# Kernel tuning notes

Measured on AMD Instinct MI355X. Metric: run time of the kernel, lower is better.

## Reference

```python
import jax, jax.numpy as jnp
import numpy as np

S = 1
R = 64
INV_T = 100.0
EVAL_STEPS = 7  # module in eval mode
EPS = 1e-6


def setup_inputs() -> dict:
    key = jax.random.key(0)
    kx, kb = jax.random.split(key)
    B, C, H, W = 8, 512, 64, 64
    x = jax.random.uniform(kx, (B, C, H, W), dtype=jnp.float32)  # non-negative input for NMF
    bases = jax.random.uniform(kb, (B * S, C // S, R), dtype=jnp.float32)
    # F.normalize(bases, dim=1): L2-normalize along D
    bases = bases / jnp.linalg.norm(bases, axis=1, keepdims=True)
    return {"x": x, "bases": bases}


def reference(x, bases):
    B, C, H, W = x.shape
    D = C // S
    N = H * W
    xf = x.reshape(B * S, D, N)  # (BS, D, N)

    # initial coefficients: softmax(inv_t * x^T @ bases)
    coef = jax.nn.softmax(INV_T * jnp.einsum('bdn,bdr->bnr', xf, bases), axis=-1)

    def mu_step(carry, _):
        bases, coef = carry
        # update coef: coef *= (x^T bases) / (coef (bases^T bases) + eps)
        num = jnp.einsum('bdn,bdr->bnr', xf, bases)            # (BS, N, R)
        gram_b = jnp.einsum('bdr,bds->brs', bases, bases)      # (BS, R, R)
        coef = coef * num / (jnp.einsum('bnr,brs->bns', coef, gram_b) + EPS)
        # update bases: bases *= (x coef) / (bases (coef^T coef) + eps)
        num_b = jnp.einsum('bdn,bnr->bdr', xf, coef)           # (BS, D, R)
        gram_c = jnp.einsum('bnr,bns->brs', coef, coef)        # (BS, R, R)
        bases = bases * num_b / (jnp.einsum('bdr,brs->bds', bases, gram_c) + EPS)
        return (bases, coef), None

    (bases, coef), _ = jax.lax.scan(mu_step, (bases, coef), None, length=EVAL_STEPS)

    # compute_coef: one extra coef multiplicative update
    num = jnp.einsum('bdn,bdr->bnr', xf, bases)
    gram_b = jnp.einsum('bdr,bds->brs', bases, bases)
    coef = coef * num / (jnp.einsum('bnr,brs->bns', coef, gram_b) + EPS)

    out = jnp.einsum('bdr,bnr->bdn', bases, coef)  # bases @ coef^T
    return out.reshape(B, C, H, W)
```

## Files before the change

kernel.cpp:

```cpp
#include <hip/hip_runtime.h>
#include <math.h>

#define BATCH 8
#define DD 512
#define NN 4096
#define RR 64
#define NSTEPS 7
#define INV_T 100.0f
#define EPSV 1e-6f

typedef __attribute__((ext_vector_type(8))) _Float16 f16x8;
typedef __attribute__((ext_vector_type(4))) _Float16 f16x4;
typedef __attribute__((ext_vector_type(4))) float f32x4;

__device__ __forceinline__ _Float16 f2h(float f) { return (_Float16)f; }

__global__ __launch_bounds__(256) void xcvt_kernel(
    const float* __restrict__ x, _Float16* __restrict__ x_h,
    _Float16* __restrict__ xT_h) {
  __shared__ _Float16 t[64][72];
  const int n0 = blockIdx.x * 64, d0 = blockIdx.y * 64, b = blockIdx.z;
  const int tid = threadIdx.x;
  const size_t xbase = (size_t)(b * DD + d0) * NN + n0;
#pragma unroll
  for (int i = 0; i < 4; ++i) {
    const int idx = tid + i * 256;
    const int row = idx >> 4, c4 = (idx & 15) * 4;
    const float4 v = *(const float4*)(x + xbase + (size_t)row * NN + c4);
    f16x4 hv = {f2h(v.x), f2h(v.y), f2h(v.z), f2h(v.w)};
    *(f16x4*)(x_h + xbase + (size_t)row * NN + c4) = hv;
    *(f16x4*)&t[row][c4] = hv;
  }
  __syncthreads();
  const size_t tbase = (size_t)(b * NN + n0) * DD + d0;
#pragma unroll
  for (int i = 0; i < 4; ++i) {
    const int idx = tid + i * 256;
    const int row = idx >> 4, c4 = (idx & 15) * 4;
    f16x4 w = {t[c4][row], t[c4 + 1][row], t[c4 + 2][row], t[c4 + 3][row]};
    *(f16x4*)(xT_h + tbase + (size_t)row * DD + c4) = w;
  }
}

__global__ __launch_bounds__(256) void bases_prep_kernel(
    const float* __restrict__ bin, float* __restrict__ bases,
    _Float16* __restrict__ bases_h, _Float16* __restrict__ basesT_h) {
  __shared__ float t[64][65];
  const int d0 = blockIdx.x * 64, b = blockIdx.y;
  const int tid = threadIdx.x;
  const size_t base = (size_t)(b * DD + d0) * RR;
#pragma unroll
  for (int i = 0; i < 4; ++i) {
    const int idx = tid + i * 256;
    const int row = idx >> 4, c4 = (idx & 15) * 4;
    const float4 v = *(const float4*)(bin + base + row * RR + c4);
    *(float4*)(bases + base + row * RR + c4) = v;
    f16x4 hv = {f2h(v.x), f2h(v.y), f2h(v.z), f2h(v.w)};
    *(f16x4*)(bases_h + base + row * RR + c4) = hv;
    t[row][c4] = v.x; t[row][c4 + 1] = v.y; t[row][c4 + 2] = v.z; t[row][c4 + 3] = v.w;
  }
  __syncthreads();
#pragma unroll
  for (int i = 0; i < 4; ++i) {
    const int idx = tid + i * 256;
    const int row = idx >> 4, c4 = (idx & 15) * 4;
    f16x4 w = {f2h(t[c4][row]), f2h(t[c4 + 1][row]), f2h(t[c4 + 2][row]),
               f2h(t[c4 + 3][row])};
    *(f16x4*)(basesT_h + (size_t)(b * RR + row) * DD + d0 + c4) = w;
  }
}

__global__ __launch_bounds__(256) void gramT_kernel(
    const _Float16* __restrict__ T, float* __restrict__ pg, int K, int ksl) {
  const int sp = blockIdx.x, b = blockIdx.y;
  const int tid = threadIdx.x;
  const int w = tid >> 6, l = tid & 63, lo = l & 15, hi = l >> 4;
  const int k0 = sp * ksl;
  const _Float16* ap = T + (size_t)(b * RR + w * 16 + lo) * K + k0 + hi * 8;
  const _Float16* bp = T + (size_t)(b * RR + lo) * K + k0 + hi * 8;
  f32x4 acc[4] = {};
  for (int ks = 0; ks < ksl; ks += 32) {
    f16x8 a = *(const f16x8*)(ap + ks);
#pragma unroll
    for (int c = 0; c < 4; ++c) {
      f16x8 bb = *(const f16x8*)(bp + (size_t)c * 16 * K + ks);
      acc[c] = __builtin_amdgcn_mfma_f32_16x16x32_f16(a, bb, acc[c], 0, 0, 0);
    }
  }
  float* op = pg + ((size_t)(b * gridDim.x + sp) * RR + w * 16 + hi * 4) * RR;
#pragma unroll
  for (int c = 0; c < 4; ++c)
#pragma unroll
    for (int r = 0; r < 4; ++r) op[r * RR + c * 16 + lo] = acc[c][r];
}

__global__ __launch_bounds__(256) void greduce2_kernel(
    const float* __restrict__ pg, int S, float* __restrict__ g32,
    _Float16* __restrict__ ghf) {
  const int idx = blockIdx.x * 256 + threadIdx.x;
  const int b = idx >> 12, e = idx & 4095;
  const float* p = pg + (size_t)(b * S) * 4096 + e;
  float s = 0.f;
  for (int c = 0; c < S; ++c) s += p[(size_t)c * 4096];
  g32[idx] = s;
  ghf[idx] = f2h(s);
}

template <int MODE>
__global__ __launch_bounds__(256) void coef_update_kernel(
    const _Float16* __restrict__ xT_h, const _Float16* __restrict__ basesT_h,
    const _Float16* __restrict__ gram_b_h, float* __restrict__ coef,
    _Float16* __restrict__ coef_h, _Float16* __restrict__ coefT_h) {
  const int nt = blockIdx.x, b = blockIdx.y;
  const int tid = threadIdx.x;
  const int w = tid >> 6, l = tid & 63, lo = l & 15, hi = l >> 4;
  const int n0 = nt * 64;

  const _Float16* ap = xT_h + (size_t)(b * NN + n0 + w * 16 + lo) * DD + hi * 8;
  const _Float16* bp = basesT_h + (size_t)(b * RR + lo) * DD + hi * 8;
  f32x4 acc[4] = {};
#pragma unroll
  for (int ks = 0; ks < 16; ++ks) {
    f16x8 a = *(const f16x8*)(ap + ks * 32);
#pragma unroll
    for (int c = 0; c < 4; ++c) {
      f16x8 bb = *(const f16x8*)(bp + (size_t)c * 16 * DD + ks * 32);
      acc[c] = __builtin_amdgcn_mfma_f32_16x16x32_f16(a, bb, acc[c], 0, 0, 0);
    }
  }

  float v[4][4];
  float* cp = coef + (size_t)(b * NN + n0 + w * 16 + hi * 4) * RR;

  if (MODE == 0) {
#pragma unroll
    for (int reg = 0; reg < 4; ++reg) {
      float m = fmaxf(fmaxf(acc[0][reg], acc[1][reg]),
                      fmaxf(acc[2][reg], acc[3][reg]));
      m = fmaxf(m, __shfl_xor(m, 1));
      m = fmaxf(m, __shfl_xor(m, 2));
      m = fmaxf(m, __shfl_xor(m, 4));
      m = fmaxf(m, __shfl_xor(m, 8));
      float s = 0.f, e[4];
#pragma unroll
      for (int c = 0; c < 4; ++c) {
        e[c] = expf(INV_T * (acc[c][reg] - m));
        s += e[c];
      }
      s += __shfl_xor(s, 1);
      s += __shfl_xor(s, 2);
      s += __shfl_xor(s, 4);
      s += __shfl_xor(s, 8);
      const float inv = 1.f / s;
#pragma unroll
      for (int c = 0; c < 4; ++c) v[c][reg] = e[c] * inv;
    }
  } else {
    const _Float16* dap = coef_h + (size_t)(b * NN + n0 + w * 16 + lo) * RR + hi * 8;
    f32x4 den[4] = {};
#pragma unroll
    for (int kk = 0; kk < 2; ++kk) {
      f16x8 a = *(const f16x8*)(dap + kk * 32);
#pragma unroll
      for (int c = 0; c < 4; ++c) {
        f16x8 g = *(const f16x8*)(gram_b_h + (size_t)(b * RR + c * 16 + lo) * RR +
                                  kk * 32 + hi * 8);
        den[c] = __builtin_amdgcn_mfma_f32_16x16x32_f16(a, g, den[c], 0, 0, 0);
      }
    }
#pragma unroll
    for (int reg = 0; reg < 4; ++reg)
#pragma unroll
      for (int c = 0; c < 4; ++c) {
        const float oldc = cp[reg * RR + c * 16 + lo];
        v[c][reg] = oldc * acc[c][reg] / (den[c][reg] + EPSV);
      }
  }

#pragma unroll
  for (int reg = 0; reg < 4; ++reg)
#pragma unroll
    for (int c = 0; c < 4; ++c) {
      cp[reg * RR + c * 16 + lo] = v[c][reg];
      coef_h[(size_t)(b * NN + n0 + w * 16 + hi * 4 + reg) * RR + c * 16 + lo] =
          f2h(v[c][reg]);
    }
#pragma unroll
  for (int c = 0; c < 4; ++c) {
    f16x4 t4 = {f2h(v[c][0]), f2h(v[c][1]), f2h(v[c][2]), f2h(v[c][3])};
    *(f16x4*)(coefT_h + (size_t)(b * RR + c * 16 + lo) * NN + n0 + w * 16 + hi * 4) = t4;
  }
}

__global__ __launch_bounds__(256) void numb_kernel(
    const _Float16* __restrict__ x_h, const _Float16* __restrict__ coefT_h,
    float* __restrict__ pnb) {
  const int kc = blockIdx.x, dt = blockIdx.y, b = blockIdx.z;
  const int tid = threadIdx.x;
  const int w = tid >> 6, l = tid & 63, lo = l & 15, hi = l >> 4;
  const _Float16* ap =
      x_h + (size_t)(b * DD + dt * 64 + w * 16 + lo) * NN + kc * 1024 + hi * 8;
  const _Float16* bp = coefT_h + (size_t)(b * RR + lo) * NN + kc * 1024 + hi * 8;
  f32x4 acc[4] = {};
#pragma unroll 4
  for (int ks = 0; ks < 32; ++ks) {
    f16x8 a = *(const f16x8*)(ap + ks * 32);
#pragma unroll
    for (int c = 0; c < 4; ++c) {
      f16x8 bb = *(const f16x8*)(bp + (size_t)c * 16 * NN + ks * 32);
      acc[c] = __builtin_amdgcn_mfma_f32_16x16x32_f16(a, bb, acc[c], 0, 0, 0);
    }
  }
  float* op = pnb + ((size_t)((b * 4 + kc) * DD) + dt * 64 + w * 16 + hi * 4) * RR;
#pragma unroll
  for (int c = 0; c < 4; ++c)
#pragma unroll
    for (int r = 0; r < 4; ++r) op[r * RR + c * 16 + lo] = acc[c][r];
}

__global__ __launch_bounds__(256) void bases_update_kernel(
    const float* __restrict__ pnb, const float* __restrict__ gram_c,
    float* __restrict__ bases, _Float16* __restrict__ bases_h,
    _Float16* __restrict__ basesT_h) {
  __shared__ float bsm[64 * 65];
  __shared__ float gs[64 * 64];
  const int dt = blockIdx.x, b = blockIdx.y;
  float* bg = bases + (size_t)(b * DD + dt * 64) * RR;
  const int tid = threadIdx.x, tx = tid & 15, ty = tid >> 4;
  for (int idx = tid; idx < 4096; idx += 256) {
    const int row = idx >> 6, cc = idx & 63;
    bsm[row * 65 + cc] = bg[row * 64 + cc];
  }
  const float* gcp = gram_c + (size_t)b * 4096;
  for (int idx = tid; idx < 1024; idx += 256)
    *(float4*)&gs[idx * 4] = *(const float4*)(gcp + idx * 4);
  __syncthreads();

  float nb[4][4];
#pragma unroll
  for (int i = 0; i < 4; ++i) {
    float4 s = make_float4(0.f, 0.f, 0.f, 0.f);
#pragma unroll
    for (int kc = 0; kc < 4; ++kc) {
      const float4 vv = *(const float4*)(pnb +
          (((size_t)b * 4 + kc) * DD + dt * 64 + ty * 4 + i) * RR + tx * 4);
      s.x += vv.x; s.y += vv.y; s.z += vv.z; s.w += vv.w;
    }
    nb[i][0] = s.x; nb[i][1] = s.y; nb[i][2] = s.z; nb[i][3] = s.w;
  }

  float den[4][4] = {};
  for (int s = 0; s < 64; ++s) {
    float a[4];
#pragma unroll
    for (int i = 0; i < 4; ++i) a[i] = bsm[(ty * 4 + i) * 65 + s];
    const float4 gv = *(float4*)&gs[s * 64 + tx * 4];
    const float g4[4] = {gv.x, gv.y, gv.z, gv.w};
#pragma unroll
    for (int i = 0; i < 4; ++i)
#pragma unroll
      for (int j = 0; j < 4; ++j) den[i][j] = fmaf(a[i], g4[j], den[i][j]);
  }

  float v[4][4];
#pragma unroll
  for (int i = 0; i < 4; ++i) {
    float4 vv;
#pragma unroll
    for (int j = 0; j < 4; ++j) {
      const float oldb = bsm[(ty * 4 + i) * 65 + tx * 4 + j];
      v[i][j] = oldb * nb[i][j] / (den[i][j] + EPSV);
    }
    vv.x = v[i][0]; vv.y = v[i][1]; vv.z = v[i][2]; vv.w = v[i][3];
    *(float4*)&bg[(ty * 4 + i) * 64 + tx * 4] = vv;
    f16x4 bv = {f2h(v[i][0]), f2h(v[i][1]), f2h(v[i][2]), f2h(v[i][3])};
    *(f16x4*)(bases_h + (size_t)(b * DD + dt * 64 + ty * 4 + i) * RR + tx * 4) = bv;
  }
#pragma unroll
  for (int j = 0; j < 4; ++j) {
    f16x4 tv = {f2h(v[0][j]), f2h(v[1][j]), f2h(v[2][j]), f2h(v[3][j])};
    *(f16x4*)(basesT_h + (size_t)(b * RR + tx * 4 + j) * DD + dt * 64 + ty * 4) = tv;
  }
}

__global__ __launch_bounds__(256) void out_kernel(
    const _Float16* __restrict__ bases_h, const _Float16* __restrict__ coef_h,
    float* __restrict__ out) {
  const int nt = blockIdx.x, dt = blockIdx.y, b = blockIdx.z;
  const int tid = threadIdx.x;
  const int w = tid >> 6, l = tid & 63, lo = l & 15, hi = l >> 4;
  const int n0 = nt * 64;
  const _Float16* ap =
      bases_h + (size_t)(b * DD + dt * 64 + w * 16 + lo) * RR + hi * 8;
  f32x4 acc[4] = {};
#pragma unroll
  for (int kk = 0; kk < 2; ++kk) {
    f16x8 a = *(const f16x8*)(ap + kk * 32);
#pragma unroll
    for (int c = 0; c < 4; ++c) {
      f16x8 bb = *(const f16x8*)(coef_h + (size_t)(b * NN + n0 + c * 16 + lo) * RR +
                                 kk * 32 + hi * 8);
      acc[c] = __builtin_amdgcn_mfma_f32_16x16x32_f16(a, bb, acc[c], 0, 0, 0);
    }
  }
  float* op = out + (size_t)(b * DD + dt * 64 + w * 16 + hi * 4) * NN + n0;
#pragma unroll
  for (int c = 0; c < 4; ++c)
#pragma unroll
    for (int r = 0; r < 4; ++r) op[(size_t)r * NN + c * 16 + lo] = acc[c][r];
}

extern "C" void kernel_launch(void* const* d_in, const int* in_sizes, int n_in,
                              void* d_out, int out_size, void* d_ws,
                              size_t ws_size, hipStream_t stream) {
  (void)in_sizes; (void)n_in; (void)out_size; (void)ws_size;
  const float* x = (const float*)d_in[0];
  const float* bases_in = (const float*)d_in[1];

  float* W = (float*)d_ws;
  size_t o = 0;
  float* coef = W + o;     o += (size_t)BATCH * NN * RR;
  float* bases = W + o;    o += (size_t)BATCH * DD * RR;
  float* gram_b32 = W + o; o += (size_t)BATCH * 4096;
  float* gram_c32 = W + o; o += (size_t)BATCH * 4096;
  float* pnb = W + o;      o += (size_t)BATCH * 4 * DD * RR;
  float* pgram = W + o;    o += (size_t)BATCH * 16 * 4096;
  _Float16* U = (_Float16*)(W + o);
  size_t u = 0;
  _Float16* coef_h = U + u;   u += (size_t)BATCH * NN * RR;
  _Float16* coefT_h = U + u;  u += (size_t)BATCH * NN * RR;
  _Float16* bases_h = U + u;  u += (size_t)BATCH * DD * RR;
  _Float16* basesT_h = U + u; u += (size_t)BATCH * DD * RR;
  _Float16* gram_b_h = U + u; u += (size_t)BATCH * 4096;
  _Float16* gram_c_h = U + u; u += (size_t)BATCH * 4096;

  _Float16* xT_h = (_Float16*)d_out;
  _Float16* x_h = xT_h + (size_t)BATCH * NN * DD;

  xcvt_kernel<<<dim3(64, 8, BATCH), 256, 0, stream>>>(x, x_h, xT_h);
  bases_prep_kernel<<<dim3(8, BATCH), 256, 0, stream>>>(bases_in, bases, bases_h,
                                                        basesT_h);
  gramT_kernel<<<dim3(4, BATCH), 256, 0, stream>>>(basesT_h, pgram, DD, 128);
  greduce2_kernel<<<128, 256, 0, stream>>>(pgram, 4, gram_b32, gram_b_h);

  coef_update_kernel<0><<<dim3(64, BATCH), 256, 0, stream>>>(
      xT_h, basesT_h, gram_b_h, coef, coef_h, coefT_h);

  for (int step = 0; step < NSTEPS; ++step) {
    coef_update_kernel<1><<<dim3(64, BATCH), 256, 0, stream>>>(
        xT_h, basesT_h, gram_b_h, coef, coef_h, coefT_h);
    gramT_kernel<<<dim3(16, BATCH), 256, 0, stream>>>(coefT_h, pgram, NN, 256);
    greduce2_kernel<<<128, 256, 0, stream>>>(pgram, 16, gram_c32, gram_c_h);
    numb_kernel<<<dim3(4, 8, BATCH), 256, 0, stream>>>(x_h, coefT_h, pnb);
    bases_update_kernel<<<dim3(8, BATCH), 256, 0, stream>>>(pnb, gram_c32, bases,
                                                            bases_h, basesT_h);
    gramT_kernel<<<dim3(4, BATCH), 256, 0, stream>>>(basesT_h, pgram, DD, 128);
    greduce2_kernel<<<128, 256, 0, stream>>>(pgram, 4, gram_b32, gram_b_h);
  }

  coef_update_kernel<1><<<dim3(64, BATCH), 256, 0, stream>>>(
      xT_h, basesT_h, gram_b_h, coef, coef_h, coefT_h);

  out_kernel<<<dim3(64, 8, BATCH), 256, 0, stream>>>(bases_h, coef_h, (float*)d_out);
}
```

Measured before the change: 638.2 us.

## Fuse NMF pipeline into a persistent cooperative kernel with grid syncs

```diff
diff --git a/kernel.cpp b/kernel.cpp
--- a/kernel.cpp
+++ b/kernel.cpp
@@ -1,5 +1,8 @@
 #include <hip/hip_runtime.h>
+#include <hip/hip_cooperative_groups.h>
 #include <math.h>
+
+namespace cg = cooperative_groups;
 
 #define BATCH 8
 #define DD 512
@@ -8,6 +11,10 @@
 #define NSTEPS 7
 #define INV_T 100.0f
 #define EPSV 1e-6f
+#define GRID 512
+#define SMEMB 24832
+#define GC_SCALE (1.0f / 1024.0f)
+#define GC_UNSCALE 1024.0f
 
 typedef __attribute__((ext_vector_type(8))) _Float16 f16x8;
 typedef __attribute__((ext_vector_type(4))) _Float16 f16x4;
@@ -15,13 +22,12 @@
 
 __device__ __forceinline__ _Float16 f2h(float f) { return (_Float16)f; }
 
-__global__ __launch_bounds__(256) void xcvt_kernel(
-    const float* __restrict__ x, _Float16* __restrict__ x_h,
-    _Float16* __restrict__ xT_h) {
-  __shared__ _Float16 t[64][72];
-  const int n0 = blockIdx.x * 64, d0 = blockIdx.y * 64, b = blockIdx.z;
-  const int tid = threadIdx.x;
+__device__ __forceinline__ void do_xcvt(const float* x, _Float16* x_h,
+                                        _Float16* xT_h, int b, int d0, int n0,
+                                        int tid, char* smem) {
+  _Float16(*t)[72] = (_Float16(*)[72])smem;
   const size_t xbase = (size_t)(b * DD + d0) * NN + n0;
+  __syncthreads();
 #pragma unroll
   for (int i = 0; i < 4; ++i) {
     const int idx = tid + i * 256;
@@ -37,24 +43,24 @@
   for (int i = 0; i < 4; ++i) {
     const int idx = tid + i * 256;
     const int row = idx >> 4, c4 = (idx & 15) * 4;
-    f16x4 w = {t[c4][row], t[c4 + 1][row], t[c4 + 2][row], t[c4 + 3][row]};
-    *(f16x4*)(xT_h + tbase + (size_t)row * DD + c4) = w;
-  }
-}
-
-__global__ __launch_bounds__(256) void bases_prep_kernel(
-    const float* __restrict__ bin, float* __restrict__ bases,
-    _Float16* __restrict__ bases_h, _Float16* __restrict__ basesT_h) {
-  __shared__ float t[64][65];
-  const int d0 = blockIdx.x * 64, b = blockIdx.y;
-  const int tid = threadIdx.x;
+    f16x4 wv = {t[c4][row], t[c4 + 1][row], t[c4 + 2][row], t[c4 + 3][row]};
+    *(f16x4*)(xT_h + tbase + (size_t)row * DD + c4) = wv;
+  }
+}
+
+__device__ __forceinline__ void do_bases_prep(const float* bin, float* bases32,
+                                              _Float16* bases_h,
+                                              _Float16* basesT_h, int b, int d0,
+                                              int tid, char* smem) {
+  float(*t)[65] = (float(*)[65])smem;
   const size_t base = (size_t)(b * DD + d0) * RR;
+  __syncthreads();
 #pragma unroll
   for (int i = 0; i < 4; ++i) {
     const int idx = tid + i * 256;
     const int row = idx >> 4, c4 = (idx & 15) * 4;
     const float4 v = *(const float4*)(bin + base + row * RR + c4);
-    *(float4*)(bases + base + row * RR + c4) = v;
+    *(float4*)(bases32 + base + row * RR + c4) = v;
     f16x4 hv = {f2h(v.x), f2h(v.y), f2h(v.z), f2h(v.w)};
     *(f16x4*)(bases_h + base + row * RR + c4) = hv;
     t[row][c4] = v.x; t[row][c4 + 1] = v.y; t[row][c4 + 2] = v.z; t[row][c4 + 3] = v.w;
@@ -64,58 +70,57 @@
   for (int i = 0; i < 4; ++i) {
     const int idx = tid + i * 256;
     const int row = idx >> 4, c4 = (idx & 15) * 4;
-    f16x4 w = {f2h(t[c4][row]), f2h(t[c4 + 1][row]), f2h(t[c4 + 2][row]),
-               f2h(t[c4 + 3][row])};
-    *(f16x4*)(basesT_h + (size_t)(b * RR + row) * DD + d0 + c4) = w;
-  }
-}
-
-__global__ __launch_bounds__(256) void gramT_kernel(
-    const _Float16* __restrict__ T, float* __restrict__ pg, int K, int ksl) {
-  const int sp = blockIdx.x, b = blockIdx.y;
-  const int tid = threadIdx.x;
-  const int w = tid >> 6, l = tid & 63, lo = l & 15, hi = l >> 4;
-  const int k0 = sp * ksl;
-  const _Float16* ap = T + (size_t)(b * RR + w * 16 + lo) * K + k0 + hi * 8;
-  const _Float16* bp = T + (size_t)(b * RR + lo) * K + k0 + hi * 8;
+    f16x4 wv = {f2h(t[c4][row]), f2h(t[c4 + 1][row]), f2h(t[c4 + 2][row]),
+                f2h(t[c4 + 3][row])};
+    *(f16x4*)(basesT_h + (size_t)(b * RR + row) * DD + d0 + c4) = wv;
+  }
+}
+
+__device__ __forceinline__ void do_gramb_init(const _Float16* basesT_h,
+                                              float* pgb, int b, int tid, int w,
+                                              int lo, int hi) {
+  const _Float16* ap = basesT_h + (size_t)(b * RR + w * 16 + lo) * DD + hi * 8;
+  const _Float16* bp = basesT_h + (size_t)(b * RR + lo) * DD + hi * 8;
   f32x4 acc[4] = {};
-  for (int ks = 0; ks < ksl; ks += 32) {
-    f16x8 a = *(const f16x8*)(ap + ks);
+#pragma unroll
+  for (int ks = 0; ks < 16; ++ks) {
+    f16x8 a = *(const f16x8*)(ap + ks * 32);
 #pragma unroll
     for (int c = 0; c < 4; ++c) {
-      f16x8 bb = *(const f16x8*)(bp + (size_t)c * 16 * K + ks);
+      f16x8 bb = *(const f16x8*)(bp + (size_t)c * 16 * DD + ks * 32);
       acc[c] = __builtin_amdgcn_mfma_f32_16x16x32_f16(a, bb, acc[c], 0, 0, 0);
     }
   }
-  float* op = pg + ((size_t)(b * gridDim.x + sp) * RR + w * 16 + hi * 4) * RR;
+  float* op = pgb + (size_t)(b * 8) * 4096;
 #pragma unroll
   for (int c = 0; c < 4; ++c)
 #pragma unroll
-    for (int r = 0; r < 4; ++r) op[r * RR + c * 16 + lo] = acc[c][r];
-}
-
-__global__ __launch_bounds__(256) void greduce2_kernel(
-    const float* __restrict__ pg, int S, float* __restrict__ g32,
-    _Float16* __restrict__ ghf) {
-  const int idx = blockIdx.x * 256 + threadIdx.x;
-  const int b = idx >> 12, e = idx & 4095;
-  const float* p = pg + (size_t)(b * S) * 4096 + e;
-  float s = 0.f;
-  for (int c = 0; c < S; ++c) s += p[(size_t)c * 4096];
-  g32[idx] = s;
-  ghf[idx] = f2h(s);
+    for (int r = 0; r < 4; ++r)
+      op[(w * 16 + hi * 4 + r) * RR + c * 16 + lo] = acc[c][r];
+  for (int sp = 1; sp < 8; ++sp)
+    for (int idx = tid; idx < 4096; idx += 256)
+      pgb[(size_t)(b * 8 + sp) * 4096 + idx] = 0.f;
 }
 
 template <int MODE>
-__global__ __launch_bounds__(256) void coef_update_kernel(
-    const _Float16* __restrict__ xT_h, const _Float16* __restrict__ basesT_h,
-    const _Float16* __restrict__ gram_b_h, float* __restrict__ coef,
-    _Float16* __restrict__ coef_h, _Float16* __restrict__ coefT_h) {
-  const int nt = blockIdx.x, b = blockIdx.y;
-  const int tid = threadIdx.x;
-  const int w = tid >> 6, l = tid & 63, lo = l & 15, hi = l >> 4;
+__device__ __forceinline__ void do_coef(const _Float16* xT_h,
+                                        const _Float16* basesT_h,
+                                        const float* pgb, float* coef32,
+                                        _Float16* coef_h, _Float16* coefT_h,
+                                        int b, int nt, int tid, int w, int lo,
+                                        int hi, char* smem) {
+  _Float16* gsm = (_Float16*)smem;
+  if (MODE == 1) {
+    __syncthreads();
+    for (int idx = tid; idx < 4096; idx += 256) {
+      float s = 0.f;
+#pragma unroll
+      for (int sp = 0; sp < 8; ++sp)
+        s += pgb[(size_t)(b * 8 + sp) * 4096 + idx];
+      gsm[idx] = f2h(s);
+    }
+  }
   const int n0 = nt * 64;
-
   const _Float16* ap = xT_h + (size_t)(b * NN + n0 + w * 16 + lo) * DD + hi * 8;
   const _Float16* bp = basesT_h + (size_t)(b * RR + lo) * DD + hi * 8;
   f32x4 acc[4] = {};
@@ -130,7 +135,7 @@
   }
 
   float v[4][4];
-  float* cp = coef + (size_t)(b * NN + n0 + w * 16 + hi * 4) * RR;
+  float* cp = coef32 + (size_t)(b * NN + n0 + w * 16 + hi * 4) * RR;
 
   if (MODE == 0) {
 #pragma unroll
@@ -156,6 +161,7 @@
       for (int c = 0; c < 4; ++c) v[c][reg] = e[c] * inv;
     }
   } else {
+    __syncthreads();
     const _Float16* dap = coef_h + (size_t)(b * NN + n0 + w * 16 + lo) * RR + hi * 8;
     f32x4 den[4] = {};
 #pragma unroll
@@ -163,9 +169,8 @@
       f16x8 a = *(const f16x8*)(dap + kk * 32);
 #pragma unroll
       for (int c = 0; c < 4; ++c) {
-        f16x8 g = *(const f16x8*)(gram_b_h + (size_t)(b * RR + c * 16 + lo) * RR +
-                                  kk * 32 + hi * 8);
-        den[c] = __builtin_amdgcn_mfma_f32_16x16x32_f16(a, g, den[c], 0, 0, 0);
+        f16x8 gv = *(const f16x8*)(gsm + (c * 16 + lo) * RR + kk * 32 + hi * 8);
+        den[c] = __builtin_amdgcn_mfma_f32_16x16x32_f16(a, gv, den[c], 0, 0, 0);
       }
     }
 #pragma unroll
@@ -192,12 +197,10 @@
   }
 }
 
-__global__ __launch_bounds__(256) void numb_kernel(
-    const _Float16* __restrict__ x_h, const _Float16* __restrict__ coefT_h,
-    float* __restrict__ pnb) {
-  const int kc = blockIdx.x, dt = blockIdx.y, b = blockIdx.z;
-  const int tid = threadIdx.x;
-  const int w = tid >> 6, l = tid & 63, lo = l & 15, hi = l >> 4;
+__device__ __forceinline__ void do_numb(const _Float16* x_h,
+                                        const _Float16* coefT_h, float* pnb,
+                                        int kc, int dt, int b, int w, int lo,
+                                        int hi) {
   const _Float16* ap =
       x_h + (size_t)(b * DD + dt * 64 + w * 16 + lo) * NN + kc * 1024 + hi * 8;
   const _Float16* bp = coefT_h + (size_t)(b * RR + lo) * NN + kc * 1024 + hi * 8;
@@ -218,22 +221,49 @@
     for (int r = 0; r < 4; ++r) op[r * RR + c * 16 + lo] = acc[c][r];
 }
 
-__global__ __launch_bounds__(256) void bases_update_kernel(
-    const float* __restrict__ pnb, const float* __restrict__ gram_c,
-    float* __restrict__ bases, _Float16* __restrict__ bases_h,
-    _Float16* __restrict__ basesT_h) {
-  __shared__ float bsm[64 * 65];
-  __shared__ float gs[64 * 64];
-  const int dt = blockIdx.x, b = blockIdx.y;
-  float* bg = bases + (size_t)(b * DD + dt * 64) * RR;
-  const int tid = threadIdx.x, tx = tid & 15, ty = tid >> 4;
+__device__ __forceinline__ void do_gramc(const _Float16* coefT_h, float* pgram,
+                                         int sp, int b, int w, int lo, int hi) {
+  const int k0 = sp * 256;
+  const _Float16* ap = coefT_h + (size_t)(b * RR + w * 16 + lo) * NN + k0 + hi * 8;
+  const _Float16* bp = coefT_h + (size_t)(b * RR + lo) * NN + k0 + hi * 8;
+  f32x4 acc[4] = {};
+#pragma unroll
+  for (int ks = 0; ks < 8; ++ks) {
+    f16x8 a = *(const f16x8*)(ap + ks * 32);
+#pragma unroll
+    for (int c = 0; c < 4; ++c) {
+      f16x8 bb = *(const f16x8*)(bp + (size_t)c * 16 * NN + ks * 32);
+      acc[c] = __builtin_amdgcn_mfma_f32_16x16x32_f16(a, bb, acc[c], 0, 0, 0);
+    }
+  }
+  float* op = pgram + ((size_t)(b * 16 + sp) * RR + w * 16 + hi * 4) * RR;
+#pragma unroll
+  for (int c = 0; c < 4; ++c)
+#pragma unroll
+    for (int r = 0; r < 4; ++r) op[r * RR + c * 16 + lo] = acc[c][r];
+}
+
+__device__ __forceinline__ void do_bases_upd(const float* pnb,
+                                             const float* pgram, float* bases32,
+                                             _Float16* bases_h,
+                                             _Float16* basesT_h, float* pgb,
+                                             int dt, int b, int tid, int tx,
+                                             int ty, char* smem) {
+  float* bsm = (float*)smem;
+  _Float16* gsh = (_Float16*)(smem + 16640);
+  float* bg = bases32 + (size_t)(b * DD + dt * 64) * RR;
+  __syncthreads();
   for (int idx = tid; idx < 4096; idx += 256) {
     const int row = idx >> 6, cc = idx & 63;
     bsm[row * 65 + cc] = bg[row * 64 + cc];
   }
-  const float* gcp = gram_c + (size_t)b * 4096;
-  for (int idx = tid; idx < 1024; idx += 256)
-    *(float4*)&gs[idx * 4] = *(const float4*)(gcp + idx * 4);
+  for (int idx = tid; idx < 4096; idx += 256) {
+    float s = 0.f;
+#pragma unroll
+    for (int sp = 0; sp < 16; ++sp)
+      s += pgram[(size_t)(b * 16 + sp) * 4096 + idx];
+    gsh[idx] = f2h(s * GC_SCALE);
+  }
   __syncthreads();
 
   float nb[4][4];
@@ -254,8 +284,8 @@
     float a[4];
 #pragma unroll
     for (int i = 0; i < 4; ++i) a[i] = bsm[(ty * 4 + i) * 65 + s];
-    const float4 gv = *(float4*)&gs[s * 64 + tx * 4];
-    const float g4[4] = {gv.x, gv.y, gv.z, gv.w};
+    const f16x4 gv = *(const f16x4*)&gsh[s * 64 + tx * 4];
+    const float g4[4] = {(float)gv[0], (float)gv[1], (float)gv[2], (float)gv[3]};
 #pragma unroll
     for (int i = 0; i < 4; ++i)
 #pragma unroll
@@ -269,7 +299,7 @@
 #pragma unroll
     for (int j = 0; j < 4; ++j) {
       const float oldb = bsm[(ty * 4 + i) * 65 + tx * 4 + j];
-      v[i][j] = oldb * nb[i][j] / (den[i][j] + EPSV);
+      v[i][j] = oldb * nb[i][j] / fmaf(den[i][j], GC_UNSCALE, EPSV);
     }
     vv.x = v[i][0]; vv.y = v[i][1]; vv.z = v[i][2]; vv.w = v[i][3];
     *(float4*)&bg[(ty * 4 + i) * 64 + tx * 4] = vv;
@@ -281,14 +311,37 @@
     f16x4 tv = {f2h(v[0][j]), f2h(v[1][j]), f2h(v[2][j]), f2h(v[3][j])};
     *(f16x4*)(basesT_h + (size_t)(b * RR + tx * 4 + j) * DD + dt * 64 + ty * 4) = tv;
   }
-}
-
-__global__ __launch_bounds__(256) void out_kernel(
-    const _Float16* __restrict__ bases_h, const _Float16* __restrict__ coef_h,
-    float* __restrict__ out) {
-  const int nt = blockIdx.x, dt = blockIdx.y, b = blockIdx.z;
-  const int tid = threadIdx.x;
-  const int w = tid >> 6, l = tid & 63, lo = l & 15, hi = l >> 4;
+  __syncthreads();
+#pragma unroll
+  for (int i = 0; i < 4; ++i)
+#pragma unroll
+    for (int j = 0; j < 4; ++j) bsm[(ty * 4 + i) * 65 + tx * 4 + j] = v[i][j];
+  __syncthreads();
+
+  float pa[4][4] = {};
+  for (int d = 0; d < 64; ++d) {
+    float a[4], bb[4];
+#pragma unroll
+    for (int i = 0; i < 4; ++i) a[i] = bsm[d * 65 + ty * 4 + i];
+#pragma unroll
+    for (int j = 0; j < 4; ++j) bb[j] = bsm[d * 65 + tx * 4 + j];
+#pragma unroll
+    for (int i = 0; i < 4; ++i)
+#pragma unroll
+      for (int j = 0; j < 4; ++j) pa[i][j] = fmaf(a[i], bb[j], pa[i][j]);
+  }
+  float* pp = pgb + (size_t)(b * 8 + dt) * 4096;
+#pragma unroll
+  for (int i = 0; i < 4; ++i) {
+    float4 vv = make_float4(pa[i][0], pa[i][1], pa[i][2], pa[i][3]);
+    *(float4*)(pp + (ty * 4 + i) * 64 + tx * 4) = vv;
+  }
+}
+
+__device__ __forceinline__ void do_out(const _Float16* bases_h,
+                                       const _Float16* coef_h, float* out,
+                                       int nt, int dt, int b, int w, int lo,
+                                       int hi) {
   const int n0 = nt * 64;
   const _Float16* ap =
       bases_h + (size_t)(b * DD + dt * 64 + w * 16 + lo) * RR + hi * 8;
@@ -308,6 +361,130 @@
   for (int c = 0; c < 4; ++c)
 #pragma unroll
     for (int r = 0; r < 4; ++r) op[(size_t)r * NN + c * 16 + lo] = acc[c][r];
+}
+
+__global__ __launch_bounds__(256, 2) void nmf_mega(const float* x,
+                                                   const float* bin, float* W,
+                                                   float* O) {
+  cg::grid_group gg = cg::this_grid();
+  float* coef32 = W;
+  float* bases32 = W + 2097152;
+  float* pnb = bases32 + 262144;
+  float* pgram = pnb + 1048576;
+  float* pgb = pgram + 524288;
+  _Float16* coef_h = (_Float16*)(pgb + 262144);
+  _Float16* coefT_h = coef_h + 2097152;
+  _Float16* bases_h = coefT_h + 2097152;
+  _Float16* basesT_h = bases_h + 262144;
+  _Float16* xT_h = (_Float16*)O;
+  _Float16* x_h = xT_h + (size_t)BATCH * NN * DD;
+
+  __shared__ __attribute__((aligned(16))) char smem[SMEMB];
+  const int g = blockIdx.x, tid = threadIdx.x;
+  const int w = tid >> 6, l = tid & 63, lo = l & 15, hi = l >> 4;
+  const int tx = tid & 15, ty = tid >> 4;
+
+  for (int u = g; u < 4160; u += GRID) {
+    if (u < 4096)
+      do_xcvt(x, x_h, xT_h, u >> 9, ((u >> 6) & 7) * 64, (u & 63) * 64, tid, smem);
+    else {
+      const int q = u - 4096;
+      do_bases_prep(bin, bases32, bases_h, basesT_h, q >> 3, (q & 7) * 64, tid, smem);
+    }
+  }
+  gg.sync();
+
+  for (int u = g; u < 520; u += GRID) {
+    if (u < 512)
+      do_coef<0>(xT_h, basesT_h, pgb, coef32, coef_h, coefT_h, u >> 6, u & 63,
+                 tid, w, lo, hi, smem);
+    else
+      do_gramb_init(basesT_h, pgb, u - 512, tid, w, lo, hi);
+  }
+  gg.sync();
+
+  for (int step = 0; step <= NSTEPS; ++step) {
+    do_coef<1>(xT_h, basesT_h, pgb, coef32, coef_h, coefT_h, g >> 6, g & 63,
+               tid, w, lo, hi, smem);
+    gg.sync();
+    if (step == NSTEPS) break;
+    if (g < 256)
+      do_numb(x_h, coefT_h, pnb, g & 3, (g >> 2) & 7, g >> 5, w, lo, hi);
+    else if (g < 384)
+      do_gramc(coefT_h, pgram, (g - 256) & 15, (g - 256) >> 4, w, lo, hi);
+    gg.sync();
+    if (g < 64)
+      do_bases_upd(pnb, pgram, bases32, bases_h, basesT_h, pgb, g & 7, g >> 3,
+                   tid, tx, ty, smem);
+    gg.sync();
+  }
+
+  for (int u = g; u < 4096; u += GRID)
+    do_out(bases_h, coef_h, O, u & 63, (u >> 6) & 7, u >> 9, w, lo, hi);
+}
+
+__global__ __launch_bounds__(256) void k_xcvt(const float* x, _Float16* x_h,
+                                              _Float16* xT_h) {
+  __shared__ __attribute__((aligned(16))) char smem[9216];
+  do_xcvt(x, x_h, xT_h, blockIdx.z, blockIdx.y * 64, blockIdx.x * 64,
+          threadIdx.x, smem);
+}
+__global__ __launch_bounds__(256) void k_bprep(const float* bin, float* b32,
+                                               _Float16* bh, _Float16* bth) {
+  __shared__ __attribute__((aligned(16))) char smem[16640];
+  do_bases_prep(bin, b32, bh, bth, blockIdx.y, blockIdx.x * 64, threadIdx.x,
+                smem);
+}
+__global__ __launch_bounds__(256) void k_init(const _Float16* xT_h,
+                                              const _Float16* basesT_h,
+                                              float* pgb, float* coef32,
+                                              _Float16* coef_h,
+                                              _Float16* coefT_h) {
+  __shared__ __attribute__((aligned(16))) char smem[8192];
+  const int tid = threadIdx.x, w = tid >> 6, l = tid & 63, lo = l & 15,
+            hi = l >> 4;
+  const int g = blockIdx.x;
+  if (g < 512)
+    do_coef<0>(xT_h, basesT_h, pgb, coef32, coef_h, coefT_h, g >> 6, g & 63,
+               tid, w, lo, hi, smem);
+  else
+    do_gramb_init(basesT_h, pgb, g - 512, tid, w, lo, hi);
+}
+__global__ __launch_bounds__(256) void k_coef1(const _Float16* xT_h,
+                                               const _Float16* basesT_h,
+                                               const float* pgb, float* coef32,
+                                               _Float16* coef_h,
+                                               _Float16* coefT_h) {
+  __shared__ __attribute__((aligned(16))) char smem[8192];
+  const int tid = threadIdx.x, w = tid >> 6, l = tid & 63, lo = l & 15,
+            hi = l >> 4;
+  do_coef<1>(xT_h, basesT_h, pgb, coef32, coef_h, coefT_h, blockIdx.x >> 6,
+             blockIdx.x & 63, tid, w, lo, hi, smem);
+}
+__global__ __launch_bounds__(256) void k_nbgc(const _Float16* x_h,
+                                              const _Float16* coefT_h,
+                                              float* pnb, float* pgram) {
+  const int tid = threadIdx.x, w = tid >> 6, l = tid & 63, lo = l & 15,
+            hi = l >> 4;
+  const int g = blockIdx.x;
+  if (g < 256)
+    do_numb(x_h, coefT_h, pnb, g & 3, (g >> 2) & 7, g >> 5, w, lo, hi);
+  else
+    do_gramc(coefT_h, pgram, (g - 256) & 15, (g - 256) >> 4, w, lo, hi);
+}
+__global__ __launch_bounds__(256) void k_bupd(const float* pnb,
+                                              const float* pgram, float* b32,
+                                              _Float16* bh, _Float16* bth,
+                                              float* pgb) {
+  __shared__ __attribute__((aligned(16))) char smem[SMEMB];
+  do_bases_upd(pnb, pgram, b32, bh, bth, pgb, blockIdx.x & 7, blockIdx.x >> 3,
+               threadIdx.x, threadIdx.x & 15, threadIdx.x >> 4, smem);
+}
+__global__ __launch_bounds__(256) void k_out(const _Float16* bh,
+                                             const _Float16* ch, float* out) {
+  const int tid = threadIdx.x, w = tid >> 6, l = tid & 63, lo = l & 15,
+            hi = l >> 4;
+  do_out(bh, ch, out, blockIdx.x, blockIdx.y, blockIdx.z, w, lo, hi);
 }
 
 extern "C" void kernel_launch(void* const* d_in, const int* in_sizes, int n_in,
@@ -315,51 +492,39 @@
                               size_t ws_size, hipStream_t stream) {
   (void)in_sizes; (void)n_in; (void)out_size; (void)ws_size;
   const float* x = (const float*)d_in[0];
-  const float* bases_in = (const float*)d_in[1];
-
+  const float* bin = (const float*)d_in[1];
   float* W = (float*)d_ws;
-  size_t o = 0;
-  float* coef = W + o;     o += (size_t)BATCH * NN * RR;
-  float* bases = W + o;    o += (size_t)BATCH * DD * RR;
-  float* gram_b32 = W + o; o += (size_t)BATCH * 4096;
-  float* gram_c32 = W + o; o += (size_t)BATCH * 4096;
-  float* pnb = W + o;      o += (size_t)BATCH * 4 * DD * RR;
-  float* pgram = W + o;    o += (size_t)BATCH * 16 * 4096;
-  _Float16* U = (_Float16*)(W + o);
-  size_t u = 0;
-  _Float16* coef_h = U + u;   u += (size_t)BATCH * NN * RR;
-  _Float16* coefT_h = U + u;  u += (size_t)BATCH * NN * RR;
-  _Float16* bases_h = U + u;  u += (size_t)BATCH * DD * RR;
-  _Float16* basesT_h = U + u; u += (size_t)BATCH * DD * RR;
-  _Float16* gram_b_h = U + u; u += (size_t)BATCH * 4096;
-  _Float16* gram_c_h = U + u; u += (size_t)BATCH * 4096;
-
-  _Float16* xT_h = (_Float16*)d_out;
-  _Float16* x_h = xT_h + (size_t)BATCH * NN * DD;
-
-  xcvt_kernel<<<dim3(64, 8, BATCH), 256, 0, stream>>>(x, x_h, xT_h);
-  bases_prep_kernel<<<dim3(8, BATCH), 256, 0, stream>>>(bases_in, bases, bases_h,
-                                                        basesT_h);
-  gramT_kernel<<<dim3(4, BATCH), 256, 0, stream>>>(basesT_h, pgram, DD, 128);
-  greduce2_kernel<<<128, 256, 0, stream>>>(pgram, 4, gram_b32, gram_b_h);
-
-  coef_update_kernel<0><<<dim3(64, BATCH), 256, 0, stream>>>(
-      xT_h, basesT_h, gram_b_h, coef, coef_h, coefT_h);
-
-  for (int step = 0; step < NSTEPS; ++step) {
-    coef_update_kernel<1><<<dim3(64, BATCH), 256, 0, stream>>>(
-        xT_h, basesT_h, gram_b_h, coef, coef_h, coefT_h);
-    gramT_kernel<<<dim3(16, BATCH), 256, 0, stream>>>(coefT_h, pgram, NN, 256);
-    greduce2_kernel<<<128, 256, 0, stream>>>(pgram, 16, gram_c32, gram_c_h);
-    numb_kernel<<<dim3(4, 8, BATCH), 256, 0, stream>>>(x_h, coefT_h, pnb);
-    bases_update_kernel<<<dim3(8, BATCH), 256, 0, stream>>>(pnb, gram_c32, bases,
-                                                            bases_h, basesT_h);
-    gramT_kernel<<<dim3(4, BATCH), 256, 0, stream>>>(basesT_h, pgram, DD, 128);
-    greduce2_kernel<<<128, 256, 0, stream>>>(pgram, 4, gram_b32, gram_b_h);
-  }
-
-  coef_update_kernel<1><<<dim3(64, BATCH), 256, 0, stream>>>(
-      xT_h, basesT_h, gram_b_h, coef, coef_h, coefT_h);
-
-  out_kernel<<<dim3(64, 8, BATCH), 256, 0, stream>>>(bases_h, coef_h, (float*)d_out);
-}
+  float* O = (float*)d_out;
+
+  void* args[] = {(void*)&x, (void*)&bin, (void*)&W, (void*)&O};
+  hipError_t err = hipLaunchCooperativeKernel((void*)nmf_mega, dim3(GRID),
+                                              dim3(256), args, 0, stream);
+  if (err != hipSuccess) {
+    (void)hipGetLastError();
+    float* coef32 = W;
+    float* bases32 = W + 2097152;
+    float* pnb = bases32 + 262144;
+    float* pgram = pnb + 1048576;
+    float* pgb = pgram + 524288;
+    _Float16* coef_h = (_Float16*)(pgb + 262144);
+    _Float16* coefT_h = coef_h + 2097152;
+    _Float16* bases_h = coefT_h + 2097152;
+    _Float16* basesT_h = bases_h + 262144;
+    _Float16* xT_h = (_Float16*)O;
+    _Float16* x_h = xT_h + (size_t)BATCH * NN * DD;
+
+    k_xcvt<<<dim3(64, 8, BATCH), 256, 0, stream>>>(x, x_h, xT_h);
+    k_bprep<<<dim3(8, BATCH), 256, 0, stream>>>(bin, bases32, bases_h, basesT_h);
+    k_init<<<520, 256, 0, stream>>>(xT_h, basesT_h, pgb, coef32, coef_h, coefT_h);
+    for (int s = 0; s < NSTEPS; ++s) {
+      k_coef1<<<512, 256, 0, stream>>>(xT_h, basesT_h, pgb, coef32, coef_h,
+                                       coefT_h);
+      k_nbgc<<<384, 256, 0, stream>>>(x_h, coefT_h, pnb, pgram);
+      k_bupd<<<64, 256, 0, stream>>>(pnb, pgram, bases32, bases_h, basesT_h,
+                                     pgb);
+    }
+    k_coef1<<<512, 256, 0, stream>>>(xT_h, basesT_h, pgb, coef32, coef_h,
+                                     coefT_h);
+    k_out<<<dim3(64, 8, BATCH), 256, 0, stream>>>(bases_h, coef_h, O);
+  }
+}
```

New measurement: 2.263 ms. +254.5%, slower.
